# Kernel tuning notes

Hardware: AMD Instinct MI355X
Metric: run time of the kernel (lower is better)

## Reference

```python
import jax, jax.numpy as jnp
import numpy as np

PROT_DIM = 128
LIG_DIM = 128
HIDDEN = 128
RBF_DIM = 16
RBF_CUTOFF = 8.0
SIGMA = 4.0
IN_DIM = PROT_DIM + LIG_DIM + 1 + 3 + RBF_DIM  # 276
N_PROT, N_LIG, N_EDGES = 40000, 10000, 1000000


def _mlp(x, w1, b1, w2, b2):
    return jax.nn.silu(x @ w1 + b1) @ w2 + b2


def setup_inputs() -> dict:
    key = jax.random.key(0)
    ks = jax.random.split(key, 16)
    s = 0.02
    return {
        "h_prot": jax.random.normal(ks[0], (N_PROT, PROT_DIM), jnp.float32),
        "h_lig": jax.random.normal(ks[1], (N_LIG, LIG_DIM), jnp.float32),
        "prot_pos": jax.random.normal(ks[2], (N_PROT, 3), jnp.float32),
        "lig_pos": jax.random.normal(ks[3], (N_LIG, 3), jnp.float32),
        "cross_edges": jax.random.randint(ks[4], (2, N_EDGES), 0, N_LIG, jnp.int32),
        "att_w1": jax.random.normal(ks[5], (IN_DIM, HIDDEN), jnp.float32) * s,
        "att_b1": jnp.zeros((HIDDEN,), jnp.float32),
        "att_w2": jax.random.normal(ks[6], (HIDDEN, 1), jnp.float32) * s,
        "att_b2": jnp.zeros((1,), jnp.float32),
        "proj_w1": jax.random.normal(ks[7], (IN_DIM, HIDDEN), jnp.float32) * s,
        "proj_b1": jnp.zeros((HIDDEN,), jnp.float32),
        "proj_w2": jax.random.normal(ks[8], (HIDDEN, LIG_DIM), jnp.float32) * s,
        "proj_b2": jnp.zeros((LIG_DIM,), jnp.float32),
        "ln_gamma": jnp.ones((LIG_DIM,), jnp.float32),
        "ln_beta": jnp.zeros((LIG_DIM,), jnp.float32),
    }


def reference(h_prot, h_lig, prot_pos, lig_pos, cross_edges,
              att_w1, att_b1, att_w2, att_b2,
              proj_w1, proj_b1, proj_w2, proj_b2,
              ln_gamma, ln_beta):
    p_idx, l_idx = cross_edges[0], cross_edges[1]
    n_lig = h_lig.shape[0]

    hp = h_prot[p_idx]            # [E, prot_dim]
    hl = h_lig[l_idx]             # [E, lig_dim]
    diff = lig_pos[l_idx] - prot_pos[p_idx]          # [E, 3]
    dist = jnp.linalg.norm(diff, axis=-1, keepdims=True)  # [E, 1]
    dir_unit = diff / (dist + 1e-8)
    centers = jnp.linspace(0.0, RBF_CUTOFF, RBF_DIM, dtype=dist.dtype)
    gamma = 1.0 / (2.0 * (RBF_CUTOFF / RBF_DIM) ** 2)
    rbf = jnp.exp(-gamma * (dist - centers) ** 2)    # [E, rbf_dim]
    cat = jnp.concatenate([hp, hl, dist, dir_unit, rbf], axis=-1)  # [E, in_dim]

    logits = _mlp(cat, att_w1, att_b1, att_w2, att_b2)[:, 0]  # [E]
    mx = jax.ops.segment_max(logits, l_idx, num_segments=n_lig)
    w = jnp.exp(logits - mx[l_idx])
    denom = jax.ops.segment_sum(w, l_idx, num_segments=n_lig)
    alpha = w / (denom[l_idx] + 1e-9)

    d = dist[:, 0]
    alpha = alpha * jnp.exp(-d * d / (2.0 * SIGMA * SIGMA))  # dist decay

    v = _mlp(cat, proj_w1, proj_b1, proj_w2, proj_b2)  # [E, lig_dim]
    agg = jax.ops.segment_sum(v * alpha[:, None], l_idx, num_segments=n_lig)

    x = h_lig + agg
    mu = jnp.mean(x, axis=-1, keepdims=True)
    var = jnp.var(x, axis=-1, keepdims=True)
    h_l_out = (x - mu) * jax.lax.rsqrt(var + 1e-5) * ln_gamma + ln_beta
    return h_prot, h_l_out
```

## Files before the change

### kernel.cpp

```cpp
#include <hip/hip_runtime.h>
#include <cstdint>


typedef float f2 __attribute__((ext_vector_type(2)));
typedef float f4 __attribute__((ext_vector_type(4)));

__device__ __forceinline__ float fast_rcp(float x) { return __builtin_amdgcn_rcpf(x); }
__device__ __forceinline__ float siluf(float x) { return x * fast_rcp(1.0f + __expf(-x)); }
__device__ __forceinline__ f2 fma2(f2 a, f2 b, f2 c) { return __builtin_elementwise_fma(a, b, c); }

template <int CTRL>
__device__ __forceinline__ float dpp_add(float x) {
  int t = __builtin_amdgcn_update_dpp(0, __builtin_bit_cast(int, x), CTRL, 0xF, 0xF, true);
  return x + __builtin_bit_cast(float, t);
}
__device__ __forceinline__ float rdlane(float x, int lane) {
  return __builtin_bit_cast(float, __builtin_amdgcn_readlane(__builtin_bit_cast(int, x), lane));
}
__device__ __forceinline__ float wave_sum(float x) {
  x = dpp_add<0xB1>(x);
  x = dpp_add<0x4E>(x);
  x = dpp_add<0x141>(x);
  x = dpp_add<0x140>(x);
  float a = rdlane(x, 0), b = rdlane(x, 16), c = rdlane(x, 32), d = rdlane(x, 48);
  return (a + b) + (c + d);
}

__global__ __launch_bounds__(256) void k_prep(
    const float4* __restrict__ hp4, float4* __restrict__ out4, int n4,
    const float* __restrict__ att_w1, const float* __restrict__ proj_w1,
    float* __restrict__ Gq,
    const int* __restrict__ l_idx, int ne, int* __restrict__ counts) {
  int i = blockIdx.x * blockDim.x + threadIdx.x;
  int stride = gridDim.x * blockDim.x;
  for (int j = i; j < n4; j += stride) out4[j] = hp4[j];
  for (int j = i; j < 40 * 128; j += stride) {
    int r = j >> 7, c = j & 127;
    int m = r >> 2, grp = r & 3;
    int lane = c >> 1, half = c & 1;
    const float* src = (grp < 2) ? att_w1 : proj_w1;
    Gq[j] = src[(256 + 2 * m + half) * 128 + 2 * lane + (grp & 1)];
  }
  for (int j = i; j < ne; j += stride) atomicAdd(&counts[l_idx[j]], 1);
}

__global__ __launch_bounds__(256) void k_tables(
    const float* __restrict__ h, int nrows,
    const float* __restrict__ Wa, const float* __restrict__ Wp,
    const float* __restrict__ ba, const float* __restrict__ bp,
    float* __restrict__ TA, float* __restrict__ TP, int interleaved) {
  __shared__ float hT[128 * 8];
  int t = threadIdx.x;
  int row0 = blockIdx.x * 8;
  for (int i = t; i < 1024; i += 256) {
    int r = i >> 7, k = i & 127;
    int gr = row0 + r;
    hT[k * 8 + r] = (gr < nrows) ? h[gr * 128 + k] : 0.0f;
  }
  __syncthreads();
  const float* W = (t < 128) ? Wa : Wp;
  const float* bias = (t < 128) ? ba : bp;
  int d = t & 127;
  float acc[8] = {0, 0, 0, 0, 0, 0, 0, 0};
  for (int k = 0; k < 128; ++k) {
    float w = W[k * 128 + d];
    const float4* h4 = reinterpret_cast<const float4*>(&hT[k * 8]);
    float4 a = h4[0], b = h4[1];
    acc[0] += a.x * w; acc[1] += a.y * w; acc[2] += a.z * w; acc[3] += a.w * w;
    acc[4] += b.x * w; acc[5] += b.y * w; acc[6] += b.z * w; acc[7] += b.w * w;
  }
  float bv = bias ? bias[d] : 0.0f;
  if (interleaved) {
    int pos = ((d >> 1) << 2) + (d & 1) + ((t < 128) ? 0 : 2);
    #pragma unroll
    for (int r = 0; r < 8; ++r) {
      int gr = row0 + r;
      if (gr < nrows) TA[(size_t)gr * 256 + pos] = acc[r] + bv;
    }
  } else {
    float* T = (t < 128) ? TA : TP;
    #pragma unroll
    for (int r = 0; r < 8; ++r) {
      int gr = row0 + r;
      if (gr < nrows) T[(size_t)gr * 128 + d] = acc[r] + bv;
    }
  }
}

__global__ __launch_bounds__(1024) void k_scan(const int* __restrict__ counts,
                                               int* __restrict__ offsets,
                                               int* __restrict__ cursor, int n) {
  __shared__ int tsum[1024];
  int t = threadIdx.x;
  int per = (n + 1023) >> 10;
  int base = t * per;
  int s = 0;
  for (int i = 0; i < per; ++i) {
    int idx = base + i;
    if (idx < n) s += counts[idx];
  }
  tsum[t] = s;
  __syncthreads();
  for (int off = 1; off < 1024; off <<= 1) {
    int v = (t >= off) ? tsum[t - off] : 0;
    __syncthreads();
    tsum[t] += v;
    __syncthreads();
  }
  int run = (t == 0) ? 0 : tsum[t - 1];
  for (int i = 0; i < per; ++i) {
    int idx = base + i;
    if (idx < n) {
      offsets[idx] = run;
      cursor[idx] = run;
      run += counts[idx];
    }
  }
}

__global__ void k_scatter(const int* __restrict__ p_idx, const int* __restrict__ l_idx, int ne,
                          int* __restrict__ cursor, int* __restrict__ sorted_p) {
  int i = blockIdx.x * blockDim.x + threadIdx.x;
  int stride = gridDim.x * blockDim.x;
  for (; i < ne; i += stride) {
    int l = l_idx[i];
    int pos = atomicAdd(&cursor[l], 1);
    sorted_p[pos] = p_idx[i];
  }
}

__global__ __launch_bounds__(256) void k_edge(
    const float* __restrict__ PAPP, const float* __restrict__ Gq,
    const float* __restrict__ LA, const float* __restrict__ LP,
    const float* __restrict__ prot_pos, const float* __restrict__ lig_pos,
    const int* __restrict__ offsets, const int* __restrict__ counts,
    const int* __restrict__ sorted_p,
    const float* __restrict__ att_w2, const float* __restrict__ att_b2,
    const float* __restrict__ proj_w2, const float* __restrict__ proj_b2,
    const float* __restrict__ h_lig, const float* __restrict__ ln_g,
    const float* __restrict__ ln_b,
    float* __restrict__ out, int np_total, int nl_total) {
  __shared__ alignas(16) float geoS[4][64][20];

  int t = threadIdx.x;
  int wave = t >> 6, lane = t & 63;
  int l = blockIdx.x * 4 + wave;
  if (l >= nl_total) return;
  int dd = 2 * lane;

  const f2* Gq2 = reinterpret_cast<const f2*>(Gq);
  f2 G2[40];
  #pragma unroll
  for (int r = 0; r < 40; ++r) G2[r] = Gq2[r * 64 + lane];

  float2 lav = *reinterpret_cast<const float2*>(&LA[(size_t)l * 128 + dd]);
  float2 lpv = *reinterpret_cast<const float2*>(&LP[(size_t)l * 128 + dd]);
  float2 wav = *reinterpret_cast<const float2*>(&att_w2[dd]);
  float la0 = lav.x, la1 = lav.y, lp0 = lpv.x, lp1 = lpv.y;
  float wa0 = wav.x, wa1 = wav.y;
  float lx = lig_pos[l * 3 + 0], ly = lig_pos[l * 3 + 1], lz = lig_pos[l * 3 + 2];
  float b2 = att_b2[0];

  int start = offsets[l];
  int cnt = counts[l];
  float acc0 = 0.0f, acc1 = 0.0f, den = 0.0f, gws = 0.0f;

  const float4* PAPP4 = reinterpret_cast<const float4*>(PAPP);

  for (int cbase = 0; cbase < cnt; cbase += 64) {
    int cc = min(64, cnt - cbase);
    float gReg = 0.0f;
    int pReg = 0;
    if (lane < cc) {
      int p = sorted_p[start + cbase + lane];
      pReg = p;
      float px = prot_pos[p * 3 + 0], py = prot_pos[p * 3 + 1], pz = prot_pos[p * 3 + 2];
      float dx = lx - px, dy = ly - py, dz = lz - pz;
      float d2r = dx * dx + dy * dy + dz * dz;
      float dist = sqrtf(d2r);
      float inv = fast_rcp(dist + 1e-8f);
      float rb[16];
      #pragma unroll
      for (int j = 0; j < 16; ++j) {
        float c = (8.0f / 15.0f) * (float)j;
        float dv = dist - c;
        rb[j] = __expf(-2.0f * dv * dv);
      }
      f4* dst = reinterpret_cast<f4*>(&geoS[wave][lane][0]);
      f4 w0; w0[0] = dist; w0[1] = dx * inv; w0[2] = dy * inv; w0[3] = dz * inv;
      f4 w1; w1[0] = rb[0]; w1[1] = rb[1]; w1[2] = rb[2]; w1[3] = rb[3];
      f4 w2; w2[0] = rb[4]; w2[1] = rb[5]; w2[2] = rb[6]; w2[3] = rb[7];
      f4 w3; w3[0] = rb[8]; w3[1] = rb[9]; w3[2] = rb[10]; w3[3] = rb[11];
      f4 w4; w4[0] = rb[12]; w4[1] = rb[13]; w4[2] = rb[14]; w4[3] = rb[15];
      dst[0] = w0; dst[1] = w1; dst[2] = w2; dst[3] = w3; dst[4] = w4;
      gReg = __expf(-d2r * (1.0f / 32.0f));
    }
    int p0 = __builtin_amdgcn_readlane(pReg, 0);
    float4 tv = PAPP4[(size_t)p0 * 64 + lane];
    for (int e = 0; e < cc; ++e) {
      int en = (e + 1 < cc) ? e + 1 : e;
      int pn = __builtin_amdgcn_readlane(pReg, en);
      float4 nt = PAPP4[(size_t)pn * 64 + lane];

      const f4* q4 = reinterpret_cast<const f4*>(&geoS[wave][e][0]);
      f2 cA0 = {0.0f, 0.0f}, cA1 = {0.0f, 0.0f};
      f2 cP0 = {0.0f, 0.0f}, cP1 = {0.0f, 0.0f};
      #pragma unroll
      for (int j = 0; j < 5; ++j) {
        f4 q = q4[j];
        f2 qlo = __builtin_shufflevector(q, q, 0, 1);
        f2 qhi = __builtin_shufflevector(q, q, 2, 3);
        cA0 = fma2(qlo, G2[8 * j + 0], cA0);
        cA1 = fma2(qlo, G2[8 * j + 1], cA1);
        cP0 = fma2(qlo, G2[8 * j + 2], cP0);
        cP1 = fma2(qlo, G2[8 * j + 3], cP1);
        cA0 = fma2(qhi, G2[8 * j + 4], cA0);
        cA1 = fma2(qhi, G2[8 * j + 5], cA1);
        cP0 = fma2(qhi, G2[8 * j + 6], cP0);
        cP1 = fma2(qhi, G2[8 * j + 7], cP1);
      }
      float a0 = (cA0.x + cA0.y) + (la0 + tv.x);
      float a1 = (cA1.x + cA1.y) + (la1 + tv.y);
      float pp0 = (cP0.x + cP0.y) + (lp0 + tv.z);
      float pp1 = (cP1.x + cP1.y) + (lp1 + tv.w);

      float part = siluf(a0) * wa0 + siluf(a1) * wa1;
      float tot = wave_sum(part);
      float w = __expf(tot + b2);
      float g = rdlane(gReg, e);
      float wg = w * g;
      acc0 = fmaf(wg, siluf(pp0), acc0);
      acc1 = fmaf(wg, siluf(pp1), acc1);
      den += w;
      gws += wg;
      tv = nt;
    }
  }

  float invd = 1.0f / (den + 1e-9f);
  float* accW = &geoS[wave][0][0];
  *reinterpret_cast<float2*>(&accW[dd]) = make_float2(acc0 * invd, acc1 * invd);
  const float2* W2_2 = reinterpret_cast<const float2*>(proj_w2);
  float agg0 = 0.0f, agg1 = 0.0f;
  #pragma unroll 4
  for (int k = 0; k < 128; k += 4) {
    float4 av = *reinterpret_cast<const float4*>(&accW[k]);
    float2 w0 = W2_2[(size_t)(k + 0) * 64 + lane];
    float2 w1 = W2_2[(size_t)(k + 1) * 64 + lane];
    float2 w2 = W2_2[(size_t)(k + 2) * 64 + lane];
    float2 w3 = W2_2[(size_t)(k + 3) * 64 + lane];
    agg0 += av.x * w0.x + av.y * w1.x + av.z * w2.x + av.w * w3.x;
    agg1 += av.x * w0.y + av.y * w1.y + av.z * w2.y + av.w * w3.y;
  }
  float gval = gws * invd;
  float2 pb2 = *reinterpret_cast<const float2*>(&proj_b2[dd]);
  float2 hl = *reinterpret_cast<const float2*>(&h_lig[(size_t)l * 128 + dd]);
  float x0 = agg0 + gval * pb2.x + hl.x;
  float x1 = agg1 + gval * pb2.y + hl.y;
  float s = x0 + x1, q = x0 * x0 + x1 * x1;
  s = wave_sum(s);
  q = wave_sum(q);
  float mu = s * (1.0f / 128.0f);
  float var = q * (1.0f / 128.0f) - mu * mu;
  float rstd = rsqrtf(var + 1e-5f);
  float2 gm = *reinterpret_cast<const float2*>(&ln_g[dd]);
  float2 bt = *reinterpret_cast<const float2*>(&ln_b[dd]);
  float2 y = make_float2((x0 - mu) * rstd * gm.x + bt.x,
                         (x1 - mu) * rstd * gm.y + bt.y);
  *reinterpret_cast<float2*>(&out[(size_t)(np_total + l) * 128 + dd]) = y;
}

extern "C" void kernel_launch(void* const* d_in, const int* in_sizes, int n_in,
                              void* d_out, int out_size, void* d_ws, size_t ws_size,
                              hipStream_t stream) {
  const float* h_prot   = (const float*)d_in[0];
  const float* h_lig    = (const float*)d_in[1];
  const float* prot_pos = (const float*)d_in[2];
  const float* lig_pos  = (const float*)d_in[3];
  const int*   edges    = (const int*)d_in[4];
  const float* att_w1   = (const float*)d_in[5];
  const float* att_b1   = (const float*)d_in[6];
  const float* att_w2   = (const float*)d_in[7];
  const float* att_b2   = (const float*)d_in[8];
  const float* proj_w1  = (const float*)d_in[9];
  const float* proj_b1  = (const float*)d_in[10];
  const float* proj_w2  = (const float*)d_in[11];
  const float* proj_b2  = (const float*)d_in[12];
  const float* ln_g     = (const float*)d_in[13];
  const float* ln_b     = (const float*)d_in[14];

  int NP = in_sizes[0] / 128;
  int NL = in_sizes[1] / 128;
  int NE = in_sizes[4] / 2;
  const int* p_idx = edges;
  const int* l_idx = edges + NE;

  float* out = (float*)d_out;

  float* PAPP = (float*)d_ws;
  float* LA = PAPP + (size_t)NP * 256;
  float* LP = LA + (size_t)NL * 128;
  float* Gq = LP + (size_t)NL * 128;
  int* counts  = (int*)(Gq + 40 * 128);
  int* offsets = counts + NL;
  int* cursor  = offsets + NL;
  int* sorted_p = cursor + NL;

  (void)hipMemsetAsync(counts, 0, (size_t)NL * sizeof(int), stream);

  k_prep<<<2048, 256, 0, stream>>>((const float4*)h_prot, (float4*)out, NP * 128 / 4,
                                   att_w1, proj_w1, Gq, l_idx, NE, counts);

  k_tables<<<(NP + 7) / 8, 256, 0, stream>>>(h_prot, NP, att_w1, proj_w1,
                                             nullptr, nullptr, PAPP, nullptr, 1);
  k_tables<<<(NL + 7) / 8, 256, 0, stream>>>(h_lig, NL, att_w1 + 128 * 128,
                                             proj_w1 + 128 * 128, att_b1, proj_b1,
                                             LA, LP, 0);

  k_scan<<<1, 1024, 0, stream>>>(counts, offsets, cursor, NL);
  k_scatter<<<4096, 256, 0, stream>>>(p_idx, l_idx, NE, cursor, sorted_p);

  k_edge<<<(NL + 3) / 4, 256, 0, stream>>>(PAPP, Gq, LA, LP, prot_pos, lig_pos,
                                           offsets, counts, sorted_p,
                                           att_w2, att_b2, proj_w2, proj_b2,
                                           h_lig, ln_g, ln_b, out, NP, NL);
}
```

Before: 554.1 us.

## Process two edges per iteration and use single-wave blocks in edge kernel

The edge loop now handles two edges at once, with two independent FMA chains and one combined dual wave reduction for both logits. This is meant to add instruction-level parallelism and halve the serialized cross-lane reduction latency per edge. Blocks shrink from four waves to one wave per ligand, so a ligand with many edges no longer holds back the other waves in its block. The cost is higher register pressure from the doubled accumulators plus masking work for odd edge counts.

```diff
diff --git a/kernel.cpp b/kernel.cpp
--- a/kernel.cpp
+++ b/kernel.cpp
@@ -24,6 +24,16 @@
   x = dpp_add<0x140>(x);
   float a = rdlane(x, 0), b = rdlane(x, 16), c = rdlane(x, 32), d = rdlane(x, 48);
   return (a + b) + (c + d);
+}
+__device__ __forceinline__ void wave_sum2(float& x, float& y) {
+  x = dpp_add<0xB1>(x);  y = dpp_add<0xB1>(y);
+  x = dpp_add<0x4E>(x);  y = dpp_add<0x4E>(y);
+  x = dpp_add<0x141>(x); y = dpp_add<0x141>(y);
+  x = dpp_add<0x140>(x); y = dpp_add<0x140>(y);
+  float a0 = rdlane(x, 0), a1 = rdlane(x, 16), a2 = rdlane(x, 32), a3 = rdlane(x, 48);
+  float b0 = rdlane(y, 0), b1 = rdlane(y, 16), b2 = rdlane(y, 32), b3 = rdlane(y, 48);
+  x = (a0 + a1) + (a2 + a3);
+  y = (b0 + b1) + (b2 + b3);
 }
 
 __global__ __launch_bounds__(256) void k_prep(
@@ -129,7 +139,7 @@
   }
 }
 
-__global__ __launch_bounds__(256) void k_edge(
+__global__ __launch_bounds__(64) void k_edge(
     const float* __restrict__ PAPP, const float* __restrict__ Gq,
     const float* __restrict__ LA, const float* __restrict__ LP,
     const float* __restrict__ prot_pos, const float* __restrict__ lig_pos,
@@ -140,11 +150,10 @@
     const float* __restrict__ h_lig, const float* __restrict__ ln_g,
     const float* __restrict__ ln_b,
     float* __restrict__ out, int np_total, int nl_total) {
-  __shared__ alignas(16) float geoS[4][64][20];
-
-  int t = threadIdx.x;
-  int wave = t >> 6, lane = t & 63;
-  int l = blockIdx.x * 4 + wave;
+  __shared__ alignas(16) float geoS[64][20];
+
+  int lane = threadIdx.x;
+  int l = blockIdx.x;
   if (l >= nl_total) return;
   int dd = 2 * lane;
 
@@ -186,7 +195,7 @@
         float dv = dist - c;
         rb[j] = __expf(-2.0f * dv * dv);
       }
-      f4* dst = reinterpret_cast<f4*>(&geoS[wave][lane][0]);
+      f4* dst = reinterpret_cast<f4*>(&geoS[lane][0]);
       f4 w0; w0[0] = dist; w0[1] = dx * inv; w0[2] = dy * inv; w0[3] = dz * inv;
       f4 w1; w1[0] = rb[0]; w1[1] = rb[1]; w1[2] = rb[2]; w1[3] = rb[3];
       f4 w2; w2[0] = rb[4]; w2[1] = rb[5]; w2[2] = rb[6]; w2[3] = rb[7];
@@ -195,50 +204,80 @@
       dst[0] = w0; dst[1] = w1; dst[2] = w2; dst[3] = w3; dst[4] = w4;
       gReg = __expf(-d2r * (1.0f / 32.0f));
     }
-    int p0 = __builtin_amdgcn_readlane(pReg, 0);
-    float4 tv = PAPP4[(size_t)p0 * 64 + lane];
-    for (int e = 0; e < cc; ++e) {
-      int en = (e + 1 < cc) ? e + 1 : e;
-      int pn = __builtin_amdgcn_readlane(pReg, en);
-      float4 nt = PAPP4[(size_t)pn * 64 + lane];
-
-      const f4* q4 = reinterpret_cast<const f4*>(&geoS[wave][e][0]);
-      f2 cA0 = {0.0f, 0.0f}, cA1 = {0.0f, 0.0f};
-      f2 cP0 = {0.0f, 0.0f}, cP1 = {0.0f, 0.0f};
+    int pA0 = __builtin_amdgcn_readlane(pReg, 0);
+    int pB0 = __builtin_amdgcn_readlane(pReg, cc > 1 ? 1 : 0);
+    float4 tvA = PAPP4[(size_t)pA0 * 64 + lane];
+    float4 tvB = PAPP4[(size_t)pB0 * 64 + lane];
+    for (int e = 0; e < cc; e += 2) {
+      int eB = (e + 1 < cc) ? e + 1 : e;
+      float maskB = (e + 1 < cc) ? 1.0f : 0.0f;
+      int iA2 = (e + 2 < cc) ? e + 2 : 0;
+      int iB2 = (e + 3 < cc) ? e + 3 : 0;
+      int pA2 = __builtin_amdgcn_readlane(pReg, iA2);
+      int pB2 = __builtin_amdgcn_readlane(pReg, iB2);
+      float4 ntA = PAPP4[(size_t)pA2 * 64 + lane];
+      float4 ntB = PAPP4[(size_t)pB2 * 64 + lane];
+
+      const f4* qA4 = reinterpret_cast<const f4*>(&geoS[e][0]);
+      const f4* qB4 = reinterpret_cast<const f4*>(&geoS[eB][0]);
+      f2 cAA0 = {0.0f, 0.0f}, cAA1 = {0.0f, 0.0f};
+      f2 cAP0 = {0.0f, 0.0f}, cAP1 = {0.0f, 0.0f};
+      f2 cBA0 = {0.0f, 0.0f}, cBA1 = {0.0f, 0.0f};
+      f2 cBP0 = {0.0f, 0.0f}, cBP1 = {0.0f, 0.0f};
       #pragma unroll
       for (int j = 0; j < 5; ++j) {
-        f4 q = q4[j];
-        f2 qlo = __builtin_shufflevector(q, q, 0, 1);
-        f2 qhi = __builtin_shufflevector(q, q, 2, 3);
-        cA0 = fma2(qlo, G2[8 * j + 0], cA0);
-        cA1 = fma2(qlo, G2[8 * j + 1], cA1);
-        cP0 = fma2(qlo, G2[8 * j + 2], cP0);
-        cP1 = fma2(qlo, G2[8 * j + 3], cP1);
-        cA0 = fma2(qhi, G2[8 * j + 4], cA0);
-        cA1 = fma2(qhi, G2[8 * j + 5], cA1);
-        cP0 = fma2(qhi, G2[8 * j + 6], cP0);
-        cP1 = fma2(qhi, G2[8 * j + 7], cP1);
+        f4 qA = qA4[j];
+        f4 qB = qB4[j];
+        f2 qAlo = __builtin_shufflevector(qA, qA, 0, 1);
+        f2 qAhi = __builtin_shufflevector(qA, qA, 2, 3);
+        f2 qBlo = __builtin_shufflevector(qB, qB, 0, 1);
+        f2 qBhi = __builtin_shufflevector(qB, qB, 2, 3);
+        cAA0 = fma2(qAlo, G2[8 * j + 0], cAA0);
+        cAA1 = fma2(qAlo, G2[8 * j + 1], cAA1);
+        cAP0 = fma2(qAlo, G2[8 * j + 2], cAP0);
+        cAP1 = fma2(qAlo, G2[8 * j + 3], cAP1);
+        cBA0 = fma2(qBlo, G2[8 * j + 0], cBA0);
+        cBA1 = fma2(qBlo, G2[8 * j + 1], cBA1);
+        cBP0 = fma2(qBlo, G2[8 * j + 2], cBP0);
+        cBP1 = fma2(qBlo, G2[8 * j + 3], cBP1);
+        cAA0 = fma2(qAhi, G2[8 * j + 4], cAA0);
+        cAA1 = fma2(qAhi, G2[8 * j + 5], cAA1);
+        cAP0 = fma2(qAhi, G2[8 * j + 6], cAP0);
+        cAP1 = fma2(qAhi, G2[8 * j + 7], cAP1);
+        cBA0 = fma2(qBhi, G2[8 * j + 4], cBA0);
+        cBA1 = fma2(qBhi, G2[8 * j + 5], cBA1);
+        cBP0 = fma2(qBhi, G2[8 * j + 6], cBP0);
+        cBP1 = fma2(qBhi, G2[8 * j + 7], cBP1);
       }
-      float a0 = (cA0.x + cA0.y) + (la0 + tv.x);
-      float a1 = (cA1.x + cA1.y) + (la1 + tv.y);
-      float pp0 = (cP0.x + cP0.y) + (lp0 + tv.z);
-      float pp1 = (cP1.x + cP1.y) + (lp1 + tv.w);
-
-      float part = siluf(a0) * wa0 + siluf(a1) * wa1;
-      float tot = wave_sum(part);
-      float w = __expf(tot + b2);
-      float g = rdlane(gReg, e);
-      float wg = w * g;
-      acc0 = fmaf(wg, siluf(pp0), acc0);
-      acc1 = fmaf(wg, siluf(pp1), acc1);
-      den += w;
-      gws += wg;
-      tv = nt;
+      float aA0 = (cAA0.x + cAA0.y) + (la0 + tvA.x);
+      float aA1 = (cAA1.x + cAA1.y) + (la1 + tvA.y);
+      float pA0v = (cAP0.x + cAP0.y) + (lp0 + tvA.z);
+      float pA1v = (cAP1.x + cAP1.y) + (lp1 + tvA.w);
+      float aB0 = (cBA0.x + cBA0.y) + (la0 + tvB.x);
+      float aB1 = (cBA1.x + cBA1.y) + (la1 + tvB.y);
+      float pB0v = (cBP0.x + cBP0.y) + (lp0 + tvB.z);
+      float pB1v = (cBP1.x + cBP1.y) + (lp1 + tvB.w);
+
+      float partA = siluf(aA0) * wa0 + siluf(aA1) * wa1;
+      float partB = siluf(aB0) * wa0 + siluf(aB1) * wa1;
+      wave_sum2(partA, partB);
+      float wA = __expf(partA + b2);
+      float wB = __expf(partB + b2) * maskB;
+      float gA = rdlane(gReg, e);
+      float gB = rdlane(gReg, eB);
+      float wgA = wA * gA, wgB = wB * gB;
+      acc0 = fmaf(wgA, siluf(pA0v), acc0);
+      acc1 = fmaf(wgA, siluf(pA1v), acc1);
+      acc0 = fmaf(wgB, siluf(pB0v), acc0);
+      acc1 = fmaf(wgB, siluf(pB1v), acc1);
+      den += wA + wB;
+      gws += wgA + wgB;
+      tvA = ntA; tvB = ntB;
     }
   }
 
   float invd = 1.0f / (den + 1e-9f);
-  float* accW = &geoS[wave][0][0];
+  float* accW = &geoS[0][0];
   *reinterpret_cast<float2*>(&accW[dd]) = make_float2(acc0 * invd, acc1 * invd);
   const float2* W2_2 = reinterpret_cast<const float2*>(proj_w2);
   float agg0 = 0.0f, agg1 = 0.0f;
@@ -258,8 +297,7 @@
   float x0 = agg0 + gval * pb2.x + hl.x;
   float x1 = agg1 + gval * pb2.y + hl.y;
   float s = x0 + x1, q = x0 * x0 + x1 * x1;
-  s = wave_sum(s);
-  q = wave_sum(q);
+  wave_sum2(s, q);
   float mu = s * (1.0f / 128.0f);
   float var = q * (1.0f / 128.0f) - mu * mu;
   float rstd = rsqrtf(var + 1e-5f);
@@ -320,8 +358,8 @@
   k_scan<<<1, 1024, 0, stream>>>(counts, offsets, cursor, NL);
   k_scatter<<<4096, 256, 0, stream>>>(p_idx, l_idx, NE, cursor, sorted_p);
 
-  k_edge<<<(NL + 3) / 4, 256, 0, stream>>>(PAPP, Gq, LA, LP, prot_pos, lig_pos,
-                                           offsets, counts, sorted_p,
-                                           att_w2, att_b2, proj_w2, proj_b2,
-                                           h_lig, ln_g, ln_b, out, NP, NL);
-}
+  k_edge<<<NL, 64, 0, stream>>>(PAPP, Gq, LA, LP, prot_pos, lig_pos,
+                                offsets, counts, sorted_p,
+                                att_w2, att_b2, proj_w2, proj_b2,
+                                h_lig, ln_g, ln_b, out, NP, NL);
+}
```

Result: faster. 535.8 us (-3.3%).
